# Optimization experiments

Measured on AMD Instinct MI355X. Metric: run time of the kernel, lower is better.

Reference implementation:

```python
import jax, jax.numpy as jnp
import numpy as np

S, B, H = 2048, 2, 2048
NP = 16            # num attention heads
HN = H // NP       # head dim = 128


def setup_inputs() -> dict:
    key = jax.random.key(0)
    k0, k1, k2 = jax.random.split(key, 3)
    hidden_states = jax.random.normal(k0, (S, B, H), dtype=jnp.float32) * 0.02
    w_qkv = jax.random.normal(k1, (3 * H, H), dtype=jnp.float32) * 0.02
    b_qkv = jnp.zeros((3 * H,), dtype=jnp.float32)
    w_dense = jax.random.normal(k2, (H, H), dtype=jnp.float32) * 0.02
    b_dense = jnp.zeros((H,), dtype=jnp.float32)
    # causal mask: True means "mask out" (strictly upper triangular)
    attention_mask = jnp.triu(jnp.ones((S, S), dtype=bool), k=1)[None, None]  # [1,1,S,S]
    return {
        "hidden_states": hidden_states,
        "attention_mask": attention_mask,
        "w_qkv": w_qkv,
        "b_qkv": b_qkv,
        "w_dense": w_dense,
        "b_dense": b_dense,
    }


def reference(hidden_states, attention_mask, w_qkv, b_qkv, w_dense, b_dense):
    s, b, h = hidden_states.shape
    # fused QKV projection (ColumnParallelLinear: y = x @ W^T + b)
    mixed = hidden_states @ w_qkv.T + b_qkv                 # [s,b,3h]
    mixed = mixed.reshape(s, b, NP, 3 * HN)
    q, k, v = jnp.split(mixed, 3, axis=-1)                  # each [s,b,np,hn]
    norm = 1.0 / jnp.sqrt(jnp.asarray(HN, hidden_states.dtype))
    # scaled QK^T -> [b,np,sq,sk]
    scores = jnp.einsum("sbnh,tbnh->bnst", q, k) * norm
    # attention_mask_func: masked_fill(mask, -10000.0)
    scores = jnp.where(attention_mask, jnp.asarray(-10000.0, scores.dtype), scores)
    # softmax in fp32 (softmax_in_fp32)
    probs = jax.nn.softmax(scores.astype(jnp.float32), axis=-1).astype(scores.dtype)
    # AV matmul -> [s,b,np,hn] -> [s,b,h]
    context = jnp.einsum("bnst,tbnh->sbnh", probs, v).reshape(s, b, h)
    # output projection (RowParallelLinear)
    out = context @ w_dense.T + b_dense
    return out
```

## Files before the change

### kernel.cpp

```cpp
#include <hip/hip_runtime.h>
#include <hip/hip_bf16.h>
#include <cstdint>
#include <cstddef>

#define SS   2048
#define BB   2
#define HH   2048
#define NHEAD 16
#define HDIM 128
#define H3   6144
#define MROWS 4096

typedef __attribute__((ext_vector_type(4))) float f32x4;
typedef __attribute__((ext_vector_type(8))) __bf16 bf16x8;
typedef __attribute__((ext_vector_type(8))) unsigned short us8;
typedef __attribute__((ext_vector_type(4))) unsigned short us4;

__device__ __forceinline__ unsigned short f2b(float f) {
    union { float f; unsigned u; } v; v.f = f;
    unsigned r = v.u + 0x7fffu + ((v.u >> 16) & 1u);
    return (unsigned short)(r >> 16);
}

__device__ __forceinline__ unsigned short f2b_hw(float f) {
    return __builtin_bit_cast(unsigned short, (__bf16)f);
}

__device__ __forceinline__ float exp2_fast(float x) {
    float r;
    asm("v_exp_f32 %0, %1" : "=v"(r) : "v"(x));
    return r;
}

__device__ __forceinline__ bf16x8 ld_b16x8(const unsigned short* p) {
    us8 u = *(const us8*)p;
    return __builtin_bit_cast(bf16x8, u);
}

__device__ __forceinline__ bf16x8 ld8_off(const unsigned short* base, int byteoff) {
    return __builtin_bit_cast(bf16x8, *(const us8*)((const char*)base + byteoff));
}

__device__ __forceinline__ int sw256(int b) { return b ^ (((b >> 8) & 7) << 4); }
__device__ __forceinline__ int sw128(int b) { return b ^ (((b >> 7) & 7) << 4); }

__device__ __forceinline__ void gload_lds16(const unsigned short* g, unsigned short* l) {
    __builtin_amdgcn_global_load_lds(
        (const __attribute__((address_space(1))) unsigned int*)g,
        (__attribute__((address_space(3))) unsigned int*)l, 16, 0, 0);
}

__global__ __launch_bounds__(256) void cvt_f32_bf16(
    const float* __restrict__ in, unsigned short* __restrict__ out, int n4)
{
    const int stride = gridDim.x * blockDim.x;
    for (int i = blockIdx.x * blockDim.x + threadIdx.x; i < n4; i += stride) {
        const float4 v = ((const float4*)in)[i];
        us4 o = { f2b_hw(v.x), f2b_hw(v.y), f2b_hw(v.z), f2b_hw(v.w) };
        ((us4*)out)[i] = o;
    }
}

__global__ __launch_bounds__(256) void transpose_v(
    const unsigned short* __restrict__ mixed,
    unsigned short* __restrict__ vt)
{
    const int st = blockIdx.x;
    const int nh = blockIdx.y;
    const int bb = blockIdx.z;
    const int tid = threadIdx.x;
    __shared__ unsigned short T[64][136];
#pragma unroll
    for (int i = 0; i < 4; ++i) {
        const int c = i * 256 + tid;
        const int sl = c >> 4, d0 = (c & 15) << 3;
        const us8 v = *(const us8*)(mixed +
            ((size_t)(st * 64 + sl) * BB + bb) * H3 + nh * 384 + 256 + d0);
        *(us8*)(&T[sl][d0]) = v;
    }
    __syncthreads();
#pragma unroll
    for (int i = 0; i < 4; ++i) {
        const int c = i * 256 + tid;
        const int d = c >> 3, sl0 = (c & 7) << 3;
        us8 o;
#pragma unroll
        for (int j = 0; j < 8; ++j) o[j] = T[sl0 + j][d];
        *(us8*)(vt + ((size_t)(bb * NHEAD + nh) * HDIM + d) * SS + st * 64 + sl0) = o;
    }
}

#define STAGE_UNIT(gp, lo)                                        \
    gload_lds16((gp) + soff[0], smem + (lo) + tid * 8);           \
    gload_lds16((gp) + soff[1], smem + (lo) + 4096 + tid * 8);

template <int BN, bool F32OUT>
__global__ __launch_bounds__(512, 2) void gemm_8ph(
    const unsigned short* __restrict__ A,
    const unsigned short* __restrict__ Bw,
    const float* __restrict__ bias,
    void* __restrict__ Cout,
    int Nv, int Kv)
{
    extern __shared__ unsigned short smem[];
    constexpr int NF     = BN / 64;
    constexpr int BUNITS = BN / 128;
    constexpr int BELEMS = BN * 64;

    const int tid  = threadIdx.x;
    const int lane = tid & 63;
    const int wave = tid >> 6;
    const int wm = wave >> 2, wn = wave & 3;
    const int bm = blockIdx.y, bn = blockIdx.x;

    const unsigned short* Ab = A  + (size_t)bm * 128 * Kv;
    const unsigned short* Bb = Bw + (size_t)bn * BN * Kv;

    int soff[2];
#pragma unroll
    for (int i = 0; i < 2; ++i) {
        const int p = (i * 512 + tid) * 16;
        const int l = p ^ (((p >> 7) & 7) << 4);
        soff[i] = (l >> 7) * Kv + ((l & 127) >> 1);
    }

    f32x4 acc[4][NF];
#pragma unroll
    for (int m = 0; m < 4; ++m)
#pragma unroll
        for (int n = 0; n < NF; ++n) acc[m][n] = (f32x4){0.f, 0.f, 0.f, 0.f};

    const int frow = lane & 15;
    const int g16  = (lane >> 4) << 4;
    const int swx  = (frow & 7) << 4;
    const int kx0  = g16 ^ swx;
    const int kx1  = (64 + g16) ^ swx;
    const int aRow = (wm * 64 + frow) * 128;
    const int bRow = 32768 + (wn * (BN / 4) + frow) * 128;

    const int NT = Kv >> 6;

    STAGE_UNIT(Ab, 0);
    STAGE_UNIT(Bb, 16384);
    STAGE_UNIT(Bb + 128 * Kv, 16384 + 8192);
    if constexpr (BUNITS == 3) { STAGE_UNIT(Bb + 256 * Kv, 16384 + 16384); }
    STAGE_UNIT(Bb + 64, 16384 + BELEMS);
    STAGE_UNIT(Bb + 128 * Kv + 64, 16384 + BELEMS + 8192);
    if constexpr (BUNITS == 3) { STAGE_UNIT(Bb + 256 * Kv + 64, 16384 + BELEMS + 16384); }
    if constexpr (BUNITS == 3) { asm volatile("s_waitcnt vmcnt(6)" ::: "memory"); }
    else                       { asm volatile("s_waitcnt vmcnt(4)" ::: "memory"); }
    __builtin_amdgcn_s_barrier();

    for (int t = 0; t < NT; ++t) {
        const int j  = t & 1;
        const int jn = j ^ 1;
        const int aj = j * 16384;
        const int bj = j * (BN * 128);
        const int cA = ((t + 1 < NT) ? (t + 1) : (NT - 1)) * 64;
        const int cB = ((t + 2 < NT) ? (t + 2) : (NT - 1)) * 64;

        bf16x8 bbf[NF][2];

        {
            bf16x8 a00 = ld8_off(smem, aj + aRow + 0 * 2048 + kx0);
            bf16x8 a01 = ld8_off(smem, aj + aRow + 0 * 2048 + kx1);
            bf16x8 a10 = ld8_off(smem, aj + aRow + 1 * 2048 + kx0);
            bf16x8 a11 = ld8_off(smem, aj + aRow + 1 * 2048 + kx1);
#pragma unroll
            for (int n = 0; n < NF; ++n) {
                bbf[n][0] = ld8_off(smem, bj + bRow + n * 2048 + kx0);
                bbf[n][1] = ld8_off(smem, bj + bRow + n * 2048 + kx1);
            }
            STAGE_UNIT(Ab + cA, jn * 8192);
            __builtin_amdgcn_s_barrier();
            __builtin_amdgcn_s_setprio(1);
#pragma unroll
            for (int n = 0; n < NF; ++n) {
                acc[0][n] = __builtin_amdgcn_mfma_f32_16x16x32_bf16(a00, bbf[n][0], acc[0][n], 0, 0, 0);
                acc[0][n] = __builtin_amdgcn_mfma_f32_16x16x32_bf16(a01, bbf[n][1], acc[0][n], 0, 0, 0);
                acc[1][n] = __builtin_amdgcn_mfma_f32_16x16x32_bf16(a10, bbf[n][0], acc[1][n], 0, 0, 0);
                acc[1][n] = __builtin_amdgcn_mfma_f32_16x16x32_bf16(a11, bbf[n][1], acc[1][n], 0, 0, 0);
            }
            __builtin_amdgcn_s_setprio(0);
        }
        {
            bf16x8 a00 = ld8_off(smem, aj + aRow + 2 * 2048 + kx0);
            bf16x8 a01 = ld8_off(smem, aj + aRow + 2 * 2048 + kx1);
            bf16x8 a10 = ld8_off(smem, aj + aRow + 3 * 2048 + kx0);
            bf16x8 a11 = ld8_off(smem, aj + aRow + 3 * 2048 + kx1);
            STAGE_UNIT(Bb + cB, 16384 + j * BELEMS);
            STAGE_UNIT(Bb + 128 * Kv + cB, 16384 + j * BELEMS + 8192);
            if constexpr (BUNITS == 3) {
                STAGE_UNIT(Bb + 256 * Kv + cB, 16384 + j * BELEMS + 16384);
            }
            __builtin_amdgcn_s_barrier();
            __builtin_amdgcn_s_setprio(1);
#pragma unroll
            for (int n = 0; n < NF; ++n) {
                acc[2][n] = __builtin_amdgcn_mfma_f32_16x16x32_bf16(a00, bbf[n][0], acc[2][n], 0, 0, 0);
                acc[2][n] = __builtin_amdgcn_mfma_f32_16x16x32_bf16(a01, bbf[n][1], acc[2][n], 0, 0, 0);
                acc[3][n] = __builtin_amdgcn_mfma_f32_16x16x32_bf16(a10, bbf[n][0], acc[3][n], 0, 0, 0);
                acc[3][n] = __builtin_amdgcn_mfma_f32_16x16x32_bf16(a11, bbf[n][1], acc[3][n], 0, 0, 0);
            }
            __builtin_amdgcn_s_setprio(0);
            if constexpr (BUNITS == 3) { asm volatile("s_waitcnt vmcnt(6)" ::: "memory"); }
            else                       { asm volatile("s_waitcnt vmcnt(4)" ::: "memory"); }
        }
    }

    const int r0 = (lane >> 4) << 2;
#pragma unroll
    for (int m = 0; m < 4; ++m) {
        const int row = bm * 128 + wm * 64 + m * 16 + r0;
#pragma unroll
        for (int n = 0; n < NF; ++n) {
            const int col = bn * BN + wn * (BN / 4) + n * 16 + frow;
            const float bv = bias[col];
            float scale = 1.0f;
            if constexpr (!F32OUT) {
                if ((col % 384) < 128)
                    scale = (float)(0.08838834764831843 * 1.4426950408889634);
            }
#pragma unroll
            for (int r = 0; r < 4; ++r) {
                const float o = (acc[m][n][r] + bv) * scale;
                if (F32OUT) ((float*)Cout)[(size_t)(row + r) * Nv + col] = o;
                else        ((unsigned short*)Cout)[(size_t)(row + r) * Nv + col] = f2b_hw(o);
            }
        }
    }
}

__global__ __launch_bounds__(256) void attn_kernel(
    const unsigned short* __restrict__ mixed,
    const unsigned short* __restrict__ vt,
    unsigned short* __restrict__ context)
{
    const int id   = blockIdx.x;
    const int c    = id & 7;
    const int k    = id >> 3;
    const int pair = k & 15;
    const int nhbb = c + 8 * (k >> 4);
    const int nh   = nhbb >> 1;
    const int bb   = nhbb & 1;

    const int tid  = threadIdx.x;
    const int lane = tid & 63;
    const int wave = tid >> 6;

    __shared__ __align__(1024) unsigned short smem[16384 + 16384 + 4096];

    const int frow = lane & 15;
    const int g16  = (lane >> 4) << 4;
    const int r0   = (lane >> 4) << 2;

    int koff[4], voff[4];
#pragma unroll
    for (int i = 0; i < 4; ++i) {
        const int p0 = (i * 256 + tid) * 16;
        const int lK = p0 ^ (((p0 >> 8) & 7) << 4);
        koff[i] = (lK >> 8) * (BB * H3) + ((lK & 255) >> 1);
        const int lV = p0 ^ (((p0 >> 7) & 7) << 4);
        voff[i] = (lV >> 7) * SS + ((lV & 127) >> 1);
    }

    const unsigned short* kg = mixed + (size_t)bb * H3 + nh * 384 + 128;
    const unsigned short* vg = vt + (size_t)(bb * NHEAD + nh) * HDIM * SS;

    char* Pb = (char*)(smem + 32768) + wave * 2048;

    bf16x8 ones;
#pragma unroll
    for (int j = 0; j < 8; ++j) ones[j] = (__bf16)1.0f;

    for (int half = 0; half < 2; ++half) {
        const int qt = half ? (31 - pair) : pair;
        const int q0 = qt * 64 + wave * 16;

        bf16x8 qf[4];
        {
            const unsigned short* qptr =
                mixed + ((size_t)(q0 + frow) * BB + bb) * H3 + nh * 384;
#pragma unroll
            for (int kk = 0; kk < 4; ++kk)
                qf[kk] = ld_b16x8(qptr + kk * 32 + ((lane >> 4) << 3));
        }

        f32x4 Oacc[8];
#pragma unroll
        for (int ct = 0; ct < 8; ++ct) Oacc[ct] = (f32x4){0.f, 0.f, 0.f, 0.f};
        f32x4 lacc = (f32x4){0.f, 0.f, 0.f, 0.f};
        float m_r[4] = {-1e30f, -1e30f, -1e30f, -1e30f};

        {
            unsigned short* Kd = smem + wave * 512;
            unsigned short* Vd = smem + 16384 + wave * 512;
#pragma unroll
            for (int i = 0; i < 4; ++i) {
                gload_lds16(kg + koff[i], Kd + i * 2048);
                gload_lds16(vg + voff[i], Vd + i * 2048);
            }
        }
        __syncthreads();

        int cur = 0;
        for (int kt = 0; kt <= qt; ++kt) {
            if (kt < qt) {
                const unsigned short* kt_g = kg + (size_t)(kt + 1) * 64 * (BB * H3);
                const unsigned short* vt_g = vg + (kt + 1) * 64;
                unsigned short* Kd = smem + (cur ^ 1) * 8192 + wave * 512;
                unsigned short* Vd = smem + 16384 + (cur ^ 1) * 8192 + wave * 512;
#pragma unroll
                for (int i = 0; i < 4; ++i) {
                    gload_lds16(kt_g + koff[i], Kd + i * 2048);
                    gload_lds16(vt_g + voff[i], Vd + i * 2048);
                }
            }

            const unsigned short* Ks = smem + cur * 8192;
            const unsigned short* Vs = smem + 16384 + cur * 8192;

            f32x4 sc4[4];
#pragma unroll
            for (int t = 0; t < 4; ++t) {
                f32x4 s = (f32x4){0.f, 0.f, 0.f, 0.f};
#pragma unroll
                for (int kk = 0; kk < 4; ++kk) {
                    bf16x8 kf = ld8_off(Ks, sw256((t * 16 + frow) * 256 + kk * 64 + g16));
                    s = __builtin_amdgcn_mfma_f32_16x16x32_bf16(qf[kk], kf, s, 0, 0, 0);
                }
                sc4[t] = s;
            }

            if (kt == qt) {
#pragma unroll
                for (int t = 0; t < 4; ++t) {
                    const int kcol = qt * 64 + t * 16 + frow;
#pragma unroll
                    for (int r = 0; r < 4; ++r)
                        if (kcol > q0 + r0 + r) sc4[t][r] = -1e30f;
                }
            }

            float pmax[4];
#pragma unroll
            for (int r = 0; r < 4; ++r)
                pmax[r] = fmaxf(fmaxf(sc4[0][r], sc4[1][r]), fmaxf(sc4[2][r], sc4[3][r]));
            bool need = false;
#pragma unroll
            for (int r = 0; r < 4; ++r) need = need || (pmax[r] > m_r[r] + 11.5f);
            if (__any(need)) {
                float tmax[4];
#pragma unroll
                for (int r = 0; r < 4; ++r) {
                    tmax[r] = pmax[r];
                    tmax[r] = fmaxf(tmax[r], __shfl_xor(tmax[r], 1, 64));
                    tmax[r] = fmaxf(tmax[r], __shfl_xor(tmax[r], 2, 64));
                    tmax[r] = fmaxf(tmax[r], __shfl_xor(tmax[r], 4, 64));
                    tmax[r] = fmaxf(tmax[r], __shfl_xor(tmax[r], 8, 64));
                }
                float a_r[4];
#pragma unroll
                for (int r = 0; r < 4; ++r) {
                    const float mnew = fmaxf(m_r[r], tmax[r]);
                    a_r[r] = exp2_fast(m_r[r] - mnew);
                    m_r[r] = mnew;
                    lacc[r] *= a_r[r];
                }
#pragma unroll
                for (int ct = 0; ct < 8; ++ct)
#pragma unroll
                    for (int r = 0; r < 4; ++r) Oacc[ct][r] *= a_r[r];
            }

#pragma unroll
            for (int t = 0; t < 4; ++t)
#pragma unroll
                for (int r = 0; r < 4; ++r)
                    *(unsigned short*)(Pb + sw128((r0 + r) * 128 + (t * 16 + frow) * 2)) =
                        f2b_hw(exp2_fast(sc4[t][r] - m_r[r]));

#pragma unroll
            for (int ks = 0; ks < 2; ++ks) {
                bf16x8 pf = ld8_off((const unsigned short*)Pb, sw128(frow * 128 + ks * 64 + g16));
                lacc = __builtin_amdgcn_mfma_f32_16x16x32_bf16(pf, ones, lacc, 0, 0, 0);
#pragma unroll
                for (int ct = 0; ct < 8; ++ct) {
                    bf16x8 vf = ld8_off(Vs, sw128((ct * 16 + frow) * 128 + ks * 64 + g16));
                    Oacc[ct] = __builtin_amdgcn_mfma_f32_16x16x32_bf16(pf, vf, Oacc[ct], 0, 0, 0);
                }
            }

            __syncthreads();
            cur ^= 1;
        }

        float rl[4];
#pragma unroll
        for (int r = 0; r < 4; ++r) rl[r] = __builtin_amdgcn_rcpf(lacc[r]);
#pragma unroll
        for (int ct = 0; ct < 8; ++ct) {
            const int d = ct * 16 + frow;
#pragma unroll
            for (int r = 0; r < 4; ++r) {
                const size_t row = (size_t)(q0 + r0 + r) * BB + bb;
                context[row * HH + nh * 128 + d] = f2b_hw(Oacc[ct][r] * rl[r]);
            }
        }
    }
}

extern "C" void kernel_launch(void* const* d_in, const int* in_sizes, int n_in,
                              void* d_out, int out_size, void* d_ws, size_t ws_size,
                              hipStream_t stream) {
    const float* hidden  = (const float*)d_in[0];
    const float* w_qkv   = (const float*)d_in[2];
    const float* b_qkv   = (const float*)d_in[3];
    const float* w_dense = (const float*)d_in[4];
    const float* b_dense = (const float*)d_in[5];
    float* out = (float*)d_out;

    unsigned short* mixed = (unsigned short*)d_ws;
    unsigned short* hb    = mixed + (size_t)MROWS * H3;
    unsigned short* wq    = hb + (size_t)MROWS * HH;
    unsigned short* wd    = wq + (size_t)H3 * HH;
    unsigned short* context = hb;
    unsigned short* vtg     = wq;

    dim3 blk(256);
    cvt_f32_bf16<<<2048, blk, 0, stream>>>(hidden, hb, (MROWS * HH) / 4);
    cvt_f32_bf16<<<2048, blk, 0, stream>>>(w_qkv, wq, (H3 * HH) / 4);
    cvt_f32_bf16<<<1024, blk, 0, stream>>>(w_dense, wd, (HH * HH) / 4);

    hipFuncSetAttribute(reinterpret_cast<const void*>(gemm_8ph<384, false>),
                        hipFuncAttributeMaxDynamicSharedMemorySize, 131072);
    gemm_8ph<384, false><<<dim3(H3 / 384, MROWS / 128), dim3(512), 131072, stream>>>(
        hb, wq, b_qkv, mixed, H3, HH);
    transpose_v<<<dim3(32, NHEAD, BB), blk, 0, stream>>>(mixed, vtg);
    attn_kernel<<<dim3(512), blk, 0, stream>>>(mixed, vtg, context);
    hipFuncSetAttribute(reinterpret_cast<const void*>(gemm_8ph<256, true>),
                        hipFuncAttributeMaxDynamicSharedMemorySize, 98304);
    gemm_8ph<256, true><<<dim3(HH / 256, MROWS / 128), dim3(512), 98304, stream>>>(
        context, wd, b_dense, out, HH, HH);
}
```

Measured before the change: 238.4 us.

## Split attention blocks per query tile and read V directly from global

Each attention block now handles a single query tile, ordered longest first, instead of a balanced pair of tiles, which doubles the grid to 1024 blocks. V is no longer staged in shared memory; each wave loads its V fragments straight from the transposed global buffer, so LDS use drops to the K double buffer plus the P scratch. The goal is more resident blocks and less LDS traffic. The cost is uncoalesced, redundant global V reads repeated by all four waves, relying on the cache, plus the load imbalance that the pairing used to hide.

```diff
diff --git a/kernel.cpp b/kernel.cpp
--- a/kernel.cpp
+++ b/kernel.cpp
@@ -236,176 +236,168 @@
     const unsigned short* __restrict__ vt,
     unsigned short* __restrict__ context)
 {
-    const int id   = blockIdx.x;
-    const int c    = id & 7;
-    const int k    = id >> 3;
-    const int pair = k & 15;
-    const int nhbb = c + 8 * (k >> 4);
-    const int nh   = nhbb >> 1;
-    const int bb   = nhbb & 1;
+    const int id     = blockIdx.x;
+    const int c      = id & 7;
+    const int k      = id >> 3;
+    const int qtslot = k & 31;
+    const int grp    = k >> 5;
+    const int qt     = 31 - qtslot;
+    const int nhbb   = c + 8 * grp;
+    const int nh     = nhbb >> 1;
+    const int bb     = nhbb & 1;
 
     const int tid  = threadIdx.x;
     const int lane = tid & 63;
     const int wave = tid >> 6;
 
-    __shared__ __align__(1024) unsigned short smem[16384 + 16384 + 4096];
+    __shared__ __align__(1024) unsigned short smem[16384 + 4096];
 
     const int frow = lane & 15;
     const int g16  = (lane >> 4) << 4;
     const int r0   = (lane >> 4) << 2;
-
-    int koff[4], voff[4];
+    const int kb8  = (lane >> 4) << 3;
+
+    int koff[4];
 #pragma unroll
     for (int i = 0; i < 4; ++i) {
         const int p0 = (i * 256 + tid) * 16;
         const int lK = p0 ^ (((p0 >> 8) & 7) << 4);
         koff[i] = (lK >> 8) * (BB * H3) + ((lK & 255) >> 1);
-        const int lV = p0 ^ (((p0 >> 7) & 7) << 4);
-        voff[i] = (lV >> 7) * SS + ((lV & 127) >> 1);
     }
 
     const unsigned short* kg = mixed + (size_t)bb * H3 + nh * 384 + 128;
     const unsigned short* vg = vt + (size_t)(bb * NHEAD + nh) * HDIM * SS;
 
-    char* Pb = (char*)(smem + 32768) + wave * 2048;
+    char* Pb = (char*)(smem + 16384) + wave * 2048;
 
     bf16x8 ones;
 #pragma unroll
     for (int j = 0; j < 8; ++j) ones[j] = (__bf16)1.0f;
 
-    for (int half = 0; half < 2; ++half) {
-        const int qt = half ? (31 - pair) : pair;
-        const int q0 = qt * 64 + wave * 16;
-
-        bf16x8 qf[4];
-        {
-            const unsigned short* qptr =
-                mixed + ((size_t)(q0 + frow) * BB + bb) * H3 + nh * 384;
-#pragma unroll
-            for (int kk = 0; kk < 4; ++kk)
-                qf[kk] = ld_b16x8(qptr + kk * 32 + ((lane >> 4) << 3));
-        }
-
-        f32x4 Oacc[8];
-#pragma unroll
-        for (int ct = 0; ct < 8; ++ct) Oacc[ct] = (f32x4){0.f, 0.f, 0.f, 0.f};
-        f32x4 lacc = (f32x4){0.f, 0.f, 0.f, 0.f};
-        float m_r[4] = {-1e30f, -1e30f, -1e30f, -1e30f};
-
-        {
-            unsigned short* Kd = smem + wave * 512;
-            unsigned short* Vd = smem + 16384 + wave * 512;
-#pragma unroll
-            for (int i = 0; i < 4; ++i) {
-                gload_lds16(kg + koff[i], Kd + i * 2048);
-                gload_lds16(vg + voff[i], Vd + i * 2048);
-            }
-        }
+    const int q0 = qt * 64 + wave * 16;
+
+    bf16x8 qf[4];
+    {
+        const unsigned short* qptr =
+            mixed + ((size_t)(q0 + frow) * BB + bb) * H3 + nh * 384;
+#pragma unroll
+        for (int kk = 0; kk < 4; ++kk)
+            qf[kk] = ld_b16x8(qptr + kk * 32 + kb8);
+    }
+
+    f32x4 Oacc[8];
+#pragma unroll
+    for (int ct = 0; ct < 8; ++ct) Oacc[ct] = (f32x4){0.f, 0.f, 0.f, 0.f};
+    f32x4 lacc = (f32x4){0.f, 0.f, 0.f, 0.f};
+    float m_r[4] = {-1e30f, -1e30f, -1e30f, -1e30f};
+
+    {
+        unsigned short* Kd = smem + wave * 512;
+#pragma unroll
+        for (int i = 0; i < 4; ++i)
+            gload_lds16(kg + koff[i], Kd + i * 2048);
+    }
+    __syncthreads();
+
+    int cur = 0;
+    for (int kt = 0; kt <= qt; ++kt) {
+        if (kt < qt) {
+            const unsigned short* kt_g = kg + (size_t)(kt + 1) * 64 * (BB * H3);
+            unsigned short* Kd = smem + (cur ^ 1) * 8192 + wave * 512;
+#pragma unroll
+            for (int i = 0; i < 4; ++i)
+                gload_lds16(kt_g + koff[i], Kd + i * 2048);
+        }
+
+        const unsigned short* Ks = smem + cur * 8192;
+        const int krow0 = kt * 64;
+
+        f32x4 sc4[4];
+#pragma unroll
+        for (int t = 0; t < 4; ++t) {
+            f32x4 s = (f32x4){0.f, 0.f, 0.f, 0.f};
+#pragma unroll
+            for (int kk = 0; kk < 4; ++kk) {
+                bf16x8 kf = ld8_off(Ks, sw256((t * 16 + frow) * 256 + kk * 64 + g16));
+                s = __builtin_amdgcn_mfma_f32_16x16x32_bf16(qf[kk], kf, s, 0, 0, 0);
+            }
+            sc4[t] = s;
+        }
+
+        if (kt == qt) {
+#pragma unroll
+            for (int t = 0; t < 4; ++t) {
+                const int kcol = qt * 64 + t * 16 + frow;
+#pragma unroll
+                for (int r = 0; r < 4; ++r)
+                    if (kcol > q0 + r0 + r) sc4[t][r] = -1e30f;
+            }
+        }
+
+        float pmax[4];
+#pragma unroll
+        for (int r = 0; r < 4; ++r)
+            pmax[r] = fmaxf(fmaxf(sc4[0][r], sc4[1][r]), fmaxf(sc4[2][r], sc4[3][r]));
+        bool need = false;
+#pragma unroll
+        for (int r = 0; r < 4; ++r) need = need || (pmax[r] > m_r[r] + 11.5f);
+        if (__any(need)) {
+            float tmax[4];
+#pragma unroll
+            for (int r = 0; r < 4; ++r) {
+                tmax[r] = pmax[r];
+                tmax[r] = fmaxf(tmax[r], __shfl_xor(tmax[r], 1, 64));
+                tmax[r] = fmaxf(tmax[r], __shfl_xor(tmax[r], 2, 64));
+                tmax[r] = fmaxf(tmax[r], __shfl_xor(tmax[r], 4, 64));
+                tmax[r] = fmaxf(tmax[r], __shfl_xor(tmax[r], 8, 64));
+            }
+            float a_r[4];
+#pragma unroll
+            for (int r = 0; r < 4; ++r) {
+                const float mnew = fmaxf(m_r[r], tmax[r]);
+                a_r[r] = exp2_fast(m_r[r] - mnew);
+                m_r[r] = mnew;
+                lacc[r] *= a_r[r];
+            }
+#pragma unroll
+            for (int ct = 0; ct < 8; ++ct)
+#pragma unroll
+                for (int r = 0; r < 4; ++r) Oacc[ct][r] *= a_r[r];
+        }
+
+#pragma unroll
+        for (int t = 0; t < 4; ++t)
+#pragma unroll
+            for (int r = 0; r < 4; ++r)
+                *(unsigned short*)(Pb + sw128((r0 + r) * 128 + (t * 16 + frow) * 2)) =
+                    f2b_hw(exp2_fast(sc4[t][r] - m_r[r]));
+
+#pragma unroll
+        for (int ks = 0; ks < 2; ++ks) {
+            bf16x8 pf = ld8_off((const unsigned short*)Pb, sw128(frow * 128 + ks * 64 + g16));
+            lacc = __builtin_amdgcn_mfma_f32_16x16x32_bf16(pf, ones, lacc, 0, 0, 0);
+#pragma unroll
+            for (int ct = 0; ct < 8; ++ct) {
+                bf16x8 vf = ld_b16x8(vg + (size_t)(ct * 16 + frow) * SS
+                                        + krow0 + ks * 32 + kb8);
+                Oacc[ct] = __builtin_amdgcn_mfma_f32_16x16x32_bf16(pf, vf, Oacc[ct], 0, 0, 0);
+            }
+        }
+
         __syncthreads();
-
-        int cur = 0;
-        for (int kt = 0; kt <= qt; ++kt) {
-            if (kt < qt) {
-                const unsigned short* kt_g = kg + (size_t)(kt + 1) * 64 * (BB * H3);
-                const unsigned short* vt_g = vg + (kt + 1) * 64;
-                unsigned short* Kd = smem + (cur ^ 1) * 8192 + wave * 512;
-                unsigned short* Vd = smem + 16384 + (cur ^ 1) * 8192 + wave * 512;
-#pragma unroll
-                for (int i = 0; i < 4; ++i) {
-                    gload_lds16(kt_g + koff[i], Kd + i * 2048);
-                    gload_lds16(vt_g + voff[i], Vd + i * 2048);
-                }
-            }
-
-            const unsigned short* Ks = smem + cur * 8192;
-            const unsigned short* Vs = smem + 16384 + cur * 8192;
-
-            f32x4 sc4[4];
-#pragma unroll
-            for (int t = 0; t < 4; ++t) {
-                f32x4 s = (f32x4){0.f, 0.f, 0.f, 0.f};
-#pragma unroll
-                for (int kk = 0; kk < 4; ++kk) {
-                    bf16x8 kf = ld8_off(Ks, sw256((t * 16 + frow) * 256 + kk * 64 + g16));
-                    s = __builtin_amdgcn_mfma_f32_16x16x32_bf16(qf[kk], kf, s, 0, 0, 0);
-                }
-                sc4[t] = s;
-            }
-
-            if (kt == qt) {
-#pragma unroll
-                for (int t = 0; t < 4; ++t) {
-                    const int kcol = qt * 64 + t * 16 + frow;
-#pragma unroll
-                    for (int r = 0; r < 4; ++r)
-                        if (kcol > q0 + r0 + r) sc4[t][r] = -1e30f;
-                }
-            }
-
-            float pmax[4];
-#pragma unroll
-            for (int r = 0; r < 4; ++r)
-                pmax[r] = fmaxf(fmaxf(sc4[0][r], sc4[1][r]), fmaxf(sc4[2][r], sc4[3][r]));
-            bool need = false;
-#pragma unroll
-            for (int r = 0; r < 4; ++r) need = need || (pmax[r] > m_r[r] + 11.5f);
-            if (__any(need)) {
-                float tmax[4];
-#pragma unroll
-                for (int r = 0; r < 4; ++r) {
-                    tmax[r] = pmax[r];
-                    tmax[r] = fmaxf(tmax[r], __shfl_xor(tmax[r], 1, 64));
-                    tmax[r] = fmaxf(tmax[r], __shfl_xor(tmax[r], 2, 64));
-                    tmax[r] = fmaxf(tmax[r], __shfl_xor(tmax[r], 4, 64));
-                    tmax[r] = fmaxf(tmax[r], __shfl_xor(tmax[r], 8, 64));
-                }
-                float a_r[4];
-#pragma unroll
-                for (int r = 0; r < 4; ++r) {
-                    const float mnew = fmaxf(m_r[r], tmax[r]);
-                    a_r[r] = exp2_fast(m_r[r] - mnew);
-                    m_r[r] = mnew;
-                    lacc[r] *= a_r[r];
-                }
-#pragma unroll
-                for (int ct = 0; ct < 8; ++ct)
-#pragma unroll
-                    for (int r = 0; r < 4; ++r) Oacc[ct][r] *= a_r[r];
-            }
-
-#pragma unroll
-            for (int t = 0; t < 4; ++t)
-#pragma unroll
-                for (int r = 0; r < 4; ++r)
-                    *(unsigned short*)(Pb + sw128((r0 + r) * 128 + (t * 16 + frow) * 2)) =
-                        f2b_hw(exp2_fast(sc4[t][r] - m_r[r]));
-
-#pragma unroll
-            for (int ks = 0; ks < 2; ++ks) {
-                bf16x8 pf = ld8_off((const unsigned short*)Pb, sw128(frow * 128 + ks * 64 + g16));
-                lacc = __builtin_amdgcn_mfma_f32_16x16x32_bf16(pf, ones, lacc, 0, 0, 0);
-#pragma unroll
-                for (int ct = 0; ct < 8; ++ct) {
-                    bf16x8 vf = ld8_off(Vs, sw128((ct * 16 + frow) * 128 + ks * 64 + g16));
-                    Oacc[ct] = __builtin_amdgcn_mfma_f32_16x16x32_bf16(pf, vf, Oacc[ct], 0, 0, 0);
-                }
-            }
-
-            __syncthreads();
-            cur ^= 1;
-        }
-
-        float rl[4];
-#pragma unroll
-        for (int r = 0; r < 4; ++r) rl[r] = __builtin_amdgcn_rcpf(lacc[r]);
-#pragma unroll
-        for (int ct = 0; ct < 8; ++ct) {
-            const int d = ct * 16 + frow;
-#pragma unroll
-            for (int r = 0; r < 4; ++r) {
-                const size_t row = (size_t)(q0 + r0 + r) * BB + bb;
-                context[row * HH + nh * 128 + d] = f2b_hw(Oacc[ct][r] * rl[r]);
-            }
+        cur ^= 1;
+    }
+
+    float rl[4];
+#pragma unroll
+    for (int r = 0; r < 4; ++r) rl[r] = __builtin_amdgcn_rcpf(lacc[r]);
+#pragma unroll
+    for (int ct = 0; ct < 8; ++ct) {
+        const int d = ct * 16 + frow;
+#pragma unroll
+        for (int r = 0; r < 4; ++r) {
+            const size_t row = (size_t)(q0 + r0 + r) * BB + bb;
+            context[row * HH + nh * 128 + d] = f2b_hw(Oacc[ct][r] * rl[r]);
         }
     }
 }
@@ -437,7 +429,7 @@
     gemm_8ph<384, false><<<dim3(H3 / 384, MROWS / 128), dim3(512), 131072, stream>>>(
         hb, wq, b_qkv, mixed, H3, HH);
     transpose_v<<<dim3(32, NHEAD, BB), blk, 0, stream>>>(mixed, vtg);
-    attn_kernel<<<dim3(512), blk, 0, stream>>>(mixed, vtg, context);
+    attn_kernel<<<dim3(1024), blk, 0, stream>>>(mixed, vtg, context);
     hipFuncSetAttribute(reinterpret_cast<const void*>(gemm_8ph<256, true>),
                         hipFuncAttributeMaxDynamicSharedMemorySize, 98304);
     gemm_8ph<256, true><<<dim3(HH / 256, MROWS / 128), dim3(512), 98304, stream>>>(
```

Result: slower. 373.4 us (+56.6%).
